# Performance work log

Hardware: AMD Instinct MI355X
Metric: run time of the kernel (lower is better)

## Reference

```python
import jax, jax.numpy as jnp
import numpy as np
from jax import lax

B, N, CIN, MID, OUT, G, H, CHILDS = 16, 1024, 256, 512, 256, 4, 1, 512


def _ln(x, g, b, eps=1e-6):
    m = x.mean(-1, keepdims=True)
    v = ((x - m) ** 2).mean(-1, keepdims=True)
    return (x - m) / jnp.sqrt(v + eps) * g + b


def _gconv(x, W, b):
    # grouped 1x1 conv1d: x [B,Cin,N], W [Cout, Cin//G], b [Cout]
    Bb, Cin, Nn = x.shape
    Cout = W.shape[0]
    xg = x.reshape(Bb, G, Cin // G, Nn)
    Wg = W.reshape(G, Cout // G, Cin // G)
    y = jnp.einsum('bgcn,goc->bgon', xg, Wg).reshape(Bb, Cout, Nn)
    return y + b[None, :, None]


def _forward(x, masks_roi1, masks_roi2, score_mask, gt_feat,
             W_att, b_att, W1, b1, W2, b2, g1, beta1, g2, beta2, Wg, bg):
    dt = x.dtype
    # gt branch
    gts = jax.nn.relu(gt_feat @ Wg + bg)  # [B,N,OUT]

    mr1 = masks_roi1 * score_mask[:, None, :]
    mr2 = masks_roi2 * score_mask[:, None, :]

    # attention logits without materializing the [B,N,N,2C] concat:
    # ft[b,i,j] = cat(x[b,j], x[b,i]);  logits = ft @ W_att + b_att
    Wq, Wk = W_att[:CIN], W_att[CIN:]
    lj = jnp.einsum('bjc,ch->bjh', x, Wq)  # query part (varies over j)
    li = jnp.einsum('bic,ch->bih', x, Wk)  # key part   (varies over i)
    attn = jax.nn.sigmoid(lj[:, None, :, :] + li[:, :, None, :] + b_att)  # [B,N,N,H]

    attn1 = attn * mr1[:, :, :, None]
    attn2 = attn * mr2[:, :, :, None]

    # torch fancy-index assign atten_mask[:,:,idces,:]=1 reduces to: any column
    # index appearing in ANY topk index set gets 1 along dim 2 for all b,i,h.
    k4, k2 = CHILDS // 4, CHILDS // 2
    a1 = jnp.moveaxis(attn1, 2, 3)  # [B,N,H,N] -> topk over last axis (= dim 2)
    a2 = jnp.moveaxis(attn2, 2, 3)
    idx1 = lax.top_k(a1, k4)[1]
    idx1m = lax.top_k(-a1, k4)[1]
    idx2 = lax.top_k(a2, k2)[1]
    idx2m = lax.top_k(-a2, k4)[1]
    all_idx = jnp.concatenate([idx1.ravel(), idx1m.ravel(), idx2.ravel(), idx2m.ravel()])
    col = jnp.zeros((N,), dtype=dt).at[all_idx].set(1.0)

    attn = attn * (mr1 + mr2)[:, :, :, None] * col[None, None, :, None]

    f = (score_mask == 0).astype(dt)  # [B,N]
    f_diag = f[:, :, None] * jnp.eye(N, dtype=dt)  # diag_embed
    atten = (attn + f_diag[:, :, :, None]) / CHILDS
    atten = jnp.transpose(atten, (0, 3, 2, 1))  # [B,H,Nj,Ni]

    x_t = jnp.transpose(x, (0, 2, 1))  # [B,CIN,N]
    o1 = jax.nn.relu(_gconv(x_t, W1, b1))  # [B,MID,N]
    o1m = jnp.matmul(o1.reshape(B, H, MID // H, N), atten).reshape(B, MID, N)
    o1m = _ln(jnp.transpose(o1m, (0, 2, 1)), g1, beta1)  # [B,N,MID]
    o1 = o1 + jnp.transpose(o1m, (0, 2, 1))

    o2 = jax.nn.relu(_gconv(o1, W2, b2))  # [B,OUT,N]
    o2m = jnp.matmul(o2.reshape(B, H, OUT // H, N), atten).reshape(B, OUT, N)
    node_feat = _ln(jnp.transpose(o2m, (0, 2, 1)), g2, beta2)  # [B,N,OUT]
    o2 = o2 + jnp.transpose(node_feat, (0, 2, 1))
    output2 = jnp.transpose(o2, (0, 2, 1))  # [B,N,OUT]
    return output2, gts, node_feat


def setup_inputs() -> dict:
    key = jax.random.key(0)
    ks = jax.random.split(key, 16)
    x = jax.random.normal(ks[0], (B, N, CIN), jnp.float32)
    masks_roi1 = (jax.random.uniform(ks[1], (B, N, N)) < 0.1).astype(jnp.float32)
    masks_roi2 = (jax.random.uniform(ks[2], (B, N, N)) < 0.1).astype(jnp.float32)
    score_mask = (jax.random.uniform(ks[3], (B, N)) < 0.8).astype(jnp.float32)
    gt_feat = jax.random.normal(ks[4], (B, N, CIN), jnp.float32)
    s = 0.05
    W_att = jax.random.normal(ks[5], (2 * CIN, H), jnp.float32) * s
    b_att = jnp.zeros((H,), jnp.float32)
    W1 = jax.random.normal(ks[6], (MID, CIN // G), jnp.float32) * s
    b1 = jax.random.normal(ks[7], (MID,), jnp.float32) * s
    W2 = jax.random.normal(ks[8], (OUT, MID // G), jnp.float32) * s
    b2 = jax.random.normal(ks[9], (OUT,), jnp.float32) * s
    g1 = jax.random.normal(ks[10], (MID,), jnp.float32) * s
    beta1 = jnp.zeros((MID,), jnp.float32)
    g2 = jax.random.normal(ks[11], (OUT,), jnp.float32) * s
    beta2 = jnp.zeros((OUT,), jnp.float32)
    Wg = jax.random.normal(ks[12], (CIN, OUT), jnp.float32) * s
    bg = jax.random.normal(ks[13], (OUT,), jnp.float32) * s
    return {"x": x, "masks_roi1": masks_roi1, "masks_roi2": masks_roi2,
            "score_mask": score_mask, "gt_feat": gt_feat,
            "W_att": W_att, "b_att": b_att, "W1": W1, "b1": b1,
            "W2": W2, "b2": b2, "g1": g1, "beta1": beta1,
            "g2": g2, "beta2": beta2, "Wg": Wg, "bg": bg}


def reference(x, masks_roi1, masks_roi2, score_mask, gt_feat,
              W_att, b_att, W1, b1, W2, b2, g1, beta1, g2, beta2, Wg, bg):
    return _forward(x, masks_roi1, masks_roi2, score_mask, gt_feat,
                    W_att, b_att, W1, b1, W2, b2, g1, beta1, g2, beta2, Wg, bg)
```

## Files before the change

kernel.cpp:

```cpp
#include <hip/hip_runtime.h>
#include <cstddef>
#include <cstdint>

#define B_ 16
#define N_ 1024
#define CIN_ 256
#define MID_ 512
#define OUT_ 256

typedef __attribute__((ext_vector_type(8))) short short8v;
typedef __attribute__((ext_vector_type(4))) float f32x4;
typedef unsigned long long ull;

__device__ __forceinline__ float sigf(float z){ return 1.f/(1.f+expf(-z)); }
__device__ __forceinline__ ushort f2bf(float f){
  uint32_t u=__float_as_uint(f);
  uint32_t r=(u + 0x7fffu + ((u>>16)&1u))>>16;
  return (ushort)r;
}
__device__ __forceinline__ float bf2f(ushort u){ return __uint_as_float(((uint32_t)u)<<16); }

__device__ __forceinline__ void async16(void* lds, const void* g){
  __builtin_amdgcn_global_load_lds(
      (const __attribute__((address_space(1))) uint32_t*)g,
      (__attribute__((address_space(3))) uint32_t*)lds,
      16, 0, 0);
}

__device__ __forceinline__ int colbit(const ull* __restrict__ cm, int j){
  return (int)((cm[((j>>8)<<2) | (j&3)] >> ((j>>2)&63)) & 1ull);
}

__global__ __launch_bounds__(256) void k_pc(const float* __restrict__ x,
    const float* __restrict__ gt, const float* __restrict__ Watt,
    float* __restrict__ lj, float* __restrict__ li,
    ushort* __restrict__ xb, ushort* __restrict__ gtb)
{
  int bid=blockIdx.x, wid=threadIdx.x>>6, lane=threadIdx.x&63;
  if(bid < 4096){
    int row = bid*4 + wid;
    float4 xv = ((const float4*)(x + (size_t)row*CIN_))[lane];
    ((ushort4*)(xb + (size_t)row*CIN_))[lane] =
        make_ushort4(f2bf(xv.x), f2bf(xv.y), f2bf(xv.z), f2bf(xv.w));
    float4 q = ((const float4*)Watt)[lane];
    float4 w = ((const float4*)(Watt + CIN_))[lane];
    float aq = xv.x*q.x+xv.y*q.y+xv.z*q.z+xv.w*q.w;
    float ak = xv.x*w.x+xv.y*w.y+xv.z*w.z+xv.w*w.w;
    #pragma unroll
    for(int off=32; off; off>>=1){ aq += __shfl_xor(aq,off); ak += __shfl_xor(ak,off); }
    if(lane==0){ lj[row]=aq; li[row]=ak; }
  } else {
    int row = (bid-4096)*4 + wid;
    float4 v = ((const float4*)(gt + (size_t)row*CIN_))[lane];
    ((ushort4*)(gtb + (size_t)row*CIN_))[lane] =
        make_ushort4(f2bf(v.x), f2bf(v.y), f2bf(v.z), f2bf(v.w));
  }
}

__global__ __launch_bounds__(256) void k_wcast(const float* __restrict__ W1,
    const float* __restrict__ W2, const float* __restrict__ Wg,
    ushort* __restrict__ W1b, ushort* __restrict__ W2b, ushort* __restrict__ WgTb)
{
  int bid=blockIdx.x, t=threadIdx.x;
  if(bid<128){ int i=bid*256+t; W1b[i]=f2bf(W1[i]); }
  else if(bid<256){ int i=(bid-128)*256+t; W2b[i]=f2bf(W2[i]); }
  else { int idx=(bid-256)*256+t; int o=idx>>8, c=idx&255; WgTb[idx]=f2bf(Wg[(size_t)c*OUT_+o]); }
}

__global__ __launch_bounds__(256) void k_colat(
    const float* __restrict__ m1, const float* __restrict__ m2,
    const float* __restrict__ sc, const float* __restrict__ lj,
    const float* __restrict__ li, const float* __restrict__ batt,
    ushort* __restrict__ Atb, ull* __restrict__ blockmask)
{
  int row = blockIdx.x; int b = row >> 10; int i = row & 1023;
  int t = threadIdx.x, lane = t&63, wid = t>>6;
  size_t base = (size_t)row*N_ + 4*t;
  float4 m1v = *(const float4*)(m1 + base);
  float4 m2v = *(const float4*)(m2 + base);
  float4 scv = *(const float4*)(sc + (b<<10) + 4*t);
  float4 ljv = *(const float4*)(lj + (b<<10) + 4*t);
  float lir = li[row], ba = batt[0];
  float fi = (sc[(b<<10)+i]==0.f)?1.f:0.f;
  float mr1[4] = {m1v.x*scv.x, m1v.y*scv.y, m1v.z*scv.z, m1v.w*scv.w};
  float mr2[4] = {m2v.x*scv.x, m2v.y*scv.y, m2v.z*scv.z, m2v.w*scv.w};
  float ljr[4] = {ljv.x,ljv.y,ljv.z,ljv.w};
  ushort o[4];
  #pragma unroll
  for(int k=0;k<4;++k){
    float v = sigf(ljr[k]+lir+ba);
    float val = v*(mr1[k]+mr2[k]);
    if(4*t+k==i) val += fi;
    o[k] = f2bf(val*(1.f/512.f));
  }
  *(ushort4*)(Atb+base) = make_ushort4(o[0],o[1],o[2],o[3]);
  ull zb1m0=__ballot(mr1[0]==0.f), zb1m1=__ballot(mr1[1]==0.f),
      zb1m2=__ballot(mr1[2]==0.f), zb1m3=__ballot(mr1[3]==0.f);
  ull zb2m0=__ballot(mr2[0]==0.f), zb2m1=__ballot(mr2[1]==0.f),
      zb2m2=__ballot(mr2[2]==0.f), zb2m3=__ballot(mr2[3]==0.f);
  int wz1 = __popcll(zb1m0)+__popcll(zb1m1)+__popcll(zb1m2)+__popcll(zb1m3);
  int wz2 = __popcll(zb2m0)+__popcll(zb2m1)+__popcll(zb2m2)+__popcll(zb2m3);
  __shared__ int wz[8];
  if(lane==0){ wz[wid]=wz1; wz[4+wid]=wz2; }
  __syncthreads();
  int pre1=0, pre2=0, Z1=0, Z2=0;
  #pragma unroll
  for(int w2=0;w2<4;++w2){
    Z1 += wz[w2]; Z2 += wz[4+w2];
    if(w2<wid){ pre1 += wz[w2]; pre2 += wz[4+w2]; }
  }
  ull lt = (1ull<<lane)-1ull;
  int r1 = pre1 + __popcll(zb1m0&lt)+__popcll(zb1m1&lt)+__popcll(zb1m2&lt)+__popcll(zb1m3&lt);
  int r2 = pre2 + __popcll(zb2m0&lt)+__popcll(zb2m1&lt)+__popcll(zb2m2&lt)+__popcll(zb2m3&lt);
  int P1 = 1024-Z1, P2 = 1024-Z2;
  bool rare = (P1>128)||(P2>256)||(Z1<128)||(Z2<128);
  bool q0,q1,q2,q3;
  if(!rare){
    int zb1=r1, zb2=r2;
    q0 = (mr1[0]!=0.f)||(zb1<128)||(mr2[0]!=0.f)||(zb2<128)||(P2+zb2<256);
    zb1 += (int)((zb1m0>>lane)&1ull); zb2 += (int)((zb2m0>>lane)&1ull);
    q1 = (mr1[1]!=0.f)||(zb1<128)||(mr2[1]!=0.f)||(zb2<128)||(P2+zb2<256);
    zb1 += (int)((zb1m1>>lane)&1ull); zb2 += (int)((zb2m1>>lane)&1ull);
    q2 = (mr1[2]!=0.f)||(zb1<128)||(mr2[2]!=0.f)||(zb2<128)||(P2+zb2<256);
    zb1 += (int)((zb1m2>>lane)&1ull); zb2 += (int)((zb2m2>>lane)&1ull);
    q3 = (mr1[3]!=0.f)||(zb1<128)||(mr2[3]!=0.f)||(zb2<128)||(P2+zb2<256);
  } else {
    const float* m1r = m1 + (size_t)row*N_;
    const float* m2r = m2 + (size_t)row*N_;
    const float* scr = sc + (b<<10);
    const float* ljp = lj + (b<<10);
    float a1v[4], a2v[4];
    #pragma unroll
    for(int k=0;k<4;++k){
      float v = sigf(ljp[4*t+k]+lir+ba);
      a1v[k]=mr1[k]*v; a2v[k]=mr2[k]*v;
    }
    int c1[4]={0,0,0,0}, c1m[4]={0,0,0,0}, c2[4]={0,0,0,0}, c2m[4]={0,0,0,0};
    for(int jp=0;jp<N_;++jp){
      float vv = sigf(ljp[jp]+lir+ba);
      float p1 = m1r[jp]*scr[jp]*vv, p2 = m2r[jp]*scr[jp]*vv;
      #pragma unroll
      for(int k=0;k<4;++k){
        bool lo = jp < 4*t+k;
        c1[k] += (p1>a1v[k])||((p1==a1v[k])&&lo);
        c1m[k]+= (p1<a1v[k])||((p1==a1v[k])&&lo);
        c2[k] += (p2>a2v[k])||((p2==a2v[k])&&lo);
        c2m[k]+= (p2<a2v[k])||((p2==a2v[k])&&lo);
      }
    }
    q0 = (c1[0]<128||c1m[0]<128||c2[0]<256||c2m[0]<128);
    q1 = (c1[1]<128||c1m[1]<128||c2[1]<256||c2m[1]<128);
    q2 = (c1[2]<128||c1m[2]<128||c2[2]<256||c2m[2]<128);
    q3 = (c1[3]<128||c1m[3]<128||c2[3]<256||c2m[3]<128);
  }
  ull bq0=__ballot(q0), bq1=__ballot(q1), bq2=__ballot(q2), bq3=__ballot(q3);
  if(lane<4){
    ull v = (lane==0)?bq0 : (lane==1)?bq1 : (lane==2)?bq2 : bq3;
    blockmask[(size_t)(wid*4+lane)*16384 + row] = v;
  }
}

__global__ __launch_bounds__(256) void k_colred(const ull* __restrict__ blockmask,
    ull* __restrict__ colmask64)
{
  int w = blockIdx.x;
  const ull* p = blockmask + (size_t)w*16384;
  ull acc = 0;
  for(int r=threadIdx.x; r<16384; r+=256) acc |= p[r];
  #pragma unroll
  for(int off=32; off; off>>=1) acc |= __shfl_xor(acc, off);
  __shared__ ull sm[4];
  int lane=threadIdx.x&63, wid=threadIdx.x>>6;
  if(lane==0) sm[wid]=acc;
  __syncthreads();
  if(threadIdx.x==0) colmask64[w] = sm[0]|sm[1]|sm[2]|sm[3];
}

template<int BM,int BN,int WR,int WC,int BK>
__global__ __launch_bounds__(256) void mgemm(
    const ushort* __restrict__ A, int lda, long long sAb, long long sAg,
    const ushort* __restrict__ Bp, int ldb, long long sBb, long long sBg,
    float* __restrict__ C, ushort* __restrict__ Cb, int ldc, long long sCb, long long sCg,
    ushort* __restrict__ CbT, long long sTb, long long sTg, int ldt,
    const ull* __restrict__ colmask, int scaleCb,
    const ushort* __restrict__ corrT, long long sQb, int ldq, const float* __restrict__ scp,
    int K, int nG,
    const float* __restrict__ biasM, int biasMG,
    const float* __restrict__ biasN, int relu)
{
  static_assert(WR*WC==4 && BM==WR*64 && BN==WC*64, "tile");
  __shared__ __align__(16) ushort As[BM*BK];
  __shared__ __align__(16) ushort Bs[BN*BK];
  int z=blockIdx.z, b=z/nG, g=z%nG;
  A  += (size_t)b*sAb + (size_t)g*sAg;
  Bp += (size_t)b*sBb + (size_t)g*sBg;
  size_t cOff = (size_t)b*sCb + (size_t)g*sCg;
  size_t tOff = (size_t)b*sTb + (size_t)g*sTg;
  int m0 = blockIdx.y*BM, n0 = blockIdx.x*BN;
  int tid=threadIdx.x, w=tid>>6, lane=tid&63;
  int la=lane&15, hi=lane>>4;
  int wr=w/WC, wc=w%WC;
  f32x4 acc[4][4] = {};
  constexpr int ISS = (BM+BN)*BK/2048;
  for(int k0=0;k0<K;k0+=BK){
    #pragma unroll
    for(int r=0;r<ISS;++r){
      int e = (r*256 + tid)*8;
      if(e < BM*BK){
        int row=e/BK, kk=e%BK;
        async16((char*)As + (size_t)e*2, A + (size_t)(m0+row)*lda + k0+kk);
      } else {
        int e2=e-BM*BK; int row=e2/BK, kk=e2%BK;
        async16((char*)Bs + (size_t)e2*2, Bp + (size_t)(n0+row)*ldb + k0+kk);
      }
    }
    __syncthreads();
    #pragma unroll
    for(int h=0;h<BK/32;++h){
      short8v af[4], bf4[4];
      #pragma unroll
      for(int i2=0;i2<4;++i2) af[i2] = *(const short8v*)&As[(wr*64+i2*16+la)*BK + h*32 + hi*8];
      #pragma unroll
      for(int j2=0;j2<4;++j2) bf4[j2] = *(const short8v*)&Bs[(wc*64+j2*16+la)*BK + h*32 + hi*8];
      #pragma unroll
      for(int i2=0;i2<4;++i2)
        #pragma unroll
        for(int j2=0;j2<4;++j2)
          acc[i2][j2] = __builtin_amdgcn_mfma_f32_16x16x32_bf16(af[i2], bf4[j2], acc[i2][j2], 0,0,0);
    }
    __syncthreads();
  }
  #pragma unroll
  for(int i2=0;i2<4;++i2){
    int row0 = m0 + wr*64 + i2*16 + hi*4;
    #pragma unroll
    for(int j2=0;j2<4;++j2){
      int col = n0 + wc*64 + j2*16 + la;
      float bn = biasN ? biasN[col] : 0.f;
      float cs = (scaleCb && !colbit(colmask, col)) ? 0.f : 1.f;
      #pragma unroll
      for(int r=0;r<4;++r){
        int row = row0 + r;
        float v = acc[i2][j2][r] + bn + (biasM ? biasM[(size_t)g*biasMG + row] : 0.f);
        if(corrT){
          if(scp[(size_t)b*1024 + row]==0.f && !colbit(colmask, row))
            v += (1.f/512.f)*bf2f(corrT[(size_t)b*sQb + (size_t)row*ldq + col]);
        }
        if(relu) v = fmaxf(v, 0.f);
        if(C)   C  [cOff + (size_t)row*ldc + col] = v;
        if(Cb)  Cb [cOff + (size_t)row*ldc + col] = f2bf(v*cs);
        if(CbT) CbT[tOff + (size_t)col*ldt + row] = f2bf(v);
      }
    }
  }
}

__global__ __launch_bounds__(256) void k_ln1(const ushort* __restrict__ o1mTb,
    const ushort* __restrict__ o1bT,
    const float* __restrict__ g1v, const float* __restrict__ be1, ushort* __restrict__ o1pb)
{
  int row=blockIdx.x, t=threadIdx.x;
  ushort2 vv = ((const ushort2*)(o1mTb + (size_t)row*MID_))[t];
  float vx=bf2f(vv.x), vy=bf2f(vv.y);
  float s=vx+vy, s2=vx*vx+vy*vy;
  for(int off=32; off; off>>=1){ s+=__shfl_down(s,off); s2+=__shfl_down(s2,off); }
  __shared__ float sm[8];
  int lane=t&63, wid=t>>6;
  if(lane==0){ sm[wid]=s; sm[4+wid]=s2; }
  __syncthreads();
  s=sm[0]+sm[1]+sm[2]+sm[3]; s2=sm[4]+sm[5]+sm[6]+sm[7];
  float mean=s*(1.f/MID_), var=s2*(1.f/MID_)-mean*mean;
  float rstd=rsqrtf(var+1e-6f);
  int m0=2*t;
  float a0=(vx-mean)*rstd*g1v[m0]+be1[m0];
  float a1=(vy-mean)*rstd*g1v[m0+1]+be1[m0+1];
  ushort2 rr = ((const ushort2*)(o1bT + (size_t)row*MID_))[t];
  ushort2 o; o.x=f2bf(a0+bf2f(rr.x)); o.y=f2bf(a1+bf2f(rr.y));
  ((ushort2*)(o1pb + (size_t)row*MID_))[t] = o;
}

__global__ __launch_bounds__(256) void k_ln2f(const ushort* __restrict__ o2mTb,
    const ushort* __restrict__ o2bT,
    const float* __restrict__ g2v, const float* __restrict__ be2,
    float* __restrict__ node, float* __restrict__ out2)
{
  int row=blockIdx.x, t=threadIdx.x;
  float v = bf2f(o2mTb[(size_t)row*OUT_ + t]);
  float s=v, s2=v*v;
  for(int off=32; off; off>>=1){ s+=__shfl_down(s,off); s2+=__shfl_down(s2,off); }
  __shared__ float sm[8];
  int lane=t&63, wid=t>>6;
  if(lane==0){ sm[wid]=s; sm[4+wid]=s2; }
  __syncthreads();
  s=sm[0]+sm[1]+sm[2]+sm[3]; s2=sm[4]+sm[5]+sm[6]+sm[7];
  float mean=s*(1.f/OUT_); float var=s2*(1.f/OUT_)-mean*mean;
  float rstd=rsqrtf(var+1e-6f);
  float nf=(v-mean)*rstd*g2v[t]+be2[t];
  size_t ro=(size_t)row*OUT_+t;
  node[ro]=nf;
  out2[ro]=nf + bf2f(o2bT[ro]);
}

extern "C" void kernel_launch(void* const* d_in, const int* in_sizes, int n_in,
                              void* d_out, int out_size, void* d_ws, size_t ws_size,
                              hipStream_t stream)
{
  const float* x    = (const float*)d_in[0];
  const float* m1   = (const float*)d_in[1];
  const float* m2   = (const float*)d_in[2];
  const float* sc   = (const float*)d_in[3];
  const float* gt   = (const float*)d_in[4];
  const float* Watt = (const float*)d_in[5];
  const float* batt = (const float*)d_in[6];
  const float* W1   = (const float*)d_in[7];
  const float* b1   = (const float*)d_in[8];
  const float* W2   = (const float*)d_in[9];
  const float* b2   = (const float*)d_in[10];
  const float* g1   = (const float*)d_in[11];
  const float* be1  = (const float*)d_in[12];
  const float* g2   = (const float*)d_in[13];
  const float* be2  = (const float*)d_in[14];
  const float* Wg   = (const float*)d_in[15];
  const float* bg   = (const float*)d_in[16];

  float* out2 = (float*)d_out;
  float* gtso = out2 + (size_t)B_*N_*OUT_;
  float* node = gtso + (size_t)B_*N_*OUT_;

  char* ws = (char*)d_ws;
  float* lj   = (float*)(ws);
  float* li   = (float*)(ws + 65536);
  ushort* W1b = (ushort*)(ws + 131072);
  ushort* W2b = (ushort*)(ws + 196608);
  ushort* WgTb= (ushort*)(ws + 262144);
  ull* colmask= (ull*)(ws + 393216);
  ull* blockmask = (ull*)(ws + 1048576);
  ushort* Atb = (ushort*)(ws + 4194304);
  ushort* xb   = (ushort*)(ws + 37748736);
  ushort* gtb  = (ushort*)(ws + 46137344);
  ushort* o2b  = xb;
  ushort* o2bT = gtb;
  ushort* o1b  = (ushort*)(ws + 54525952);
  ushort* o1pb = o1b;
  ushort* o1bT = (ushort*)(ws + 71303168);
  ushort* o2mTb= (ushort*)(ws + 71303168);
  ushort* o1mTb= (ushort*)(ws + 88080384);

  k_pc    <<<dim3(8192),dim3(256),0,stream>>>(x, gt, Watt, lj, li, xb, gtb);
  k_wcast <<<dim3(512),dim3(256),0,stream>>>(W1, W2, Wg, W1b, W2b, WgTb);
  k_colat <<<dim3(B_*N_),dim3(256),0,stream>>>(m1,m2,sc,lj,li,batt,Atb,blockmask);
  k_colred<<<dim3(16),dim3(256),0,stream>>>(blockmask, colmask);

  mgemm<128,128,2,2,64><<<dim3(2,128,1),256,0,stream>>>(
      gtb, CIN_, 0,0,
      WgTb, CIN_, 0,0,
      gtso, (ushort*)0, OUT_, 0,0,
      (ushort*)0, 0,0,0,
      (ull*)0, 0, (ushort*)0, 0,0, (float*)0,
      CIN_, 1, nullptr,0, bg, 1);

  mgemm<128,128,2,2,64><<<dim3(8,1,B_*4),256,0,stream>>>(
      W1b, 64, 0, (long long)128*64,
      xb, CIN_, (long long)N_*CIN_, 64,
      (float*)0, o1b, N_, (long long)MID_*N_, (long long)128*N_,
      o1bT, (long long)N_*MID_, 128, MID_,
      colmask, 1, (ushort*)0, 0,0, (float*)0,
      64, 4, b1, 128, nullptr, 1);

  mgemm<128,128,2,2,64><<<dim3(4,8,B_),256,0,stream>>>(
      Atb, N_, (long long)N_*N_, 0,
      o1b, N_, (long long)MID_*N_, 0,
      (float*)0, o1mTb, MID_, (long long)N_*MID_, 0,
      (ushort*)0, 0,0,0,
      colmask, 0, o1bT, (long long)N_*MID_, MID_, sc,
      N_, 1, nullptr,0, nullptr, 0);

  k_ln1<<<dim3(B_*N_),256,0,stream>>>(o1mTb, o1bT, g1, be1, o1pb);

  mgemm<64,256,1,4,64><<<dim3(4,1,B_*4),256,0,stream>>>(
      W2b, 128, 0, (long long)64*128,
      o1pb, MID_, (long long)N_*MID_, 128,
      (float*)0, o2b, N_, (long long)OUT_*N_, (long long)64*N_,
      o2bT, (long long)N_*OUT_, 64, OUT_,
      colmask, 1, (ushort*)0, 0,0, (float*)0,
      128, 4, b2, 64, nullptr, 1);

  mgemm<128,128,2,2,64><<<dim3(2,8,B_),256,0,stream>>>(
      Atb, N_, (long long)N_*N_, 0,
      o2b, N_, (long long)OUT_*N_, 0,
      (float*)0, o2mTb, OUT_, (long long)N_*OUT_, 0,
      (ushort*)0, 0,0,0,
      colmask, 0, o2bT, (long long)N_*OUT_, OUT_, sc,
      N_, 1, nullptr,0, nullptr, 0);

  k_ln2f<<<dim3(B_*N_),256,0,stream>>>(o2mTb, o2bT, g2, be2, node, out2);
}
```

Before: 425.5 us.

## Stage transposed GEMM stores through LDS and precompute column/row correction factors

The transposed bf16 output of the two grouped-conv GEMMs is now staged in shared memory and written out as coalesced 16-byte rows, replacing strided 2-byte scatter stores. A small kernel precomputes per-column scale and per-row correction factors so the GEMM epilogue skips bitmask decoding and the conditional corrT reads. The sigmoid also uses hardware exp2/rcp intrinsics. This adds a launch and an extra sync, and uses more LDS in the transposing variants.

```diff
diff --git a/kernel.cpp b/kernel.cpp
--- a/kernel.cpp
+++ b/kernel.cpp
@@ -12,7 +12,10 @@
 typedef __attribute__((ext_vector_type(4))) float f32x4;
 typedef unsigned long long ull;
 
-__device__ __forceinline__ float sigf(float z){ return 1.f/(1.f+expf(-z)); }
+__device__ __forceinline__ float sigf(float z){
+  float e = __builtin_amdgcn_exp2f(-z*1.44269504f);
+  return __builtin_amdgcn_rcpf(1.f+e);
+}
 __device__ __forceinline__ ushort f2bf(float f){
   uint32_t u=__float_as_uint(f);
   uint32_t r=(u + 0x7fffu + ((u>>16)&1u))>>16;
@@ -176,21 +179,36 @@
   if(threadIdx.x==0) colmask64[w] = sm[0]|sm[1]|sm[2]|sm[3];
 }
 
-template<int BM,int BN,int WR,int WC,int BK>
+__global__ __launch_bounds__(256) void k_fcorr(const ull* __restrict__ colmask,
+    const float* __restrict__ sc, float* __restrict__ fcorr, float* __restrict__ colscale)
+{
+  int i = blockIdx.x*256 + threadIdx.x;
+  int j = i & 1023;
+  int cb = colbit(colmask, j);
+  fcorr[i] = (sc[i]==0.f && !cb) ? (1.f/512.f) : 0.f;
+  if(i < 1024) colscale[i] = cb ? 1.f : 0.f;
+}
+
+template<int BM,int BN,int WR,int WC,int BK,int TRT>
 __global__ __launch_bounds__(256) void mgemm(
     const ushort* __restrict__ A, int lda, long long sAb, long long sAg,
     const ushort* __restrict__ Bp, int ldb, long long sBb, long long sBg,
     float* __restrict__ C, ushort* __restrict__ Cb, int ldc, long long sCb, long long sCg,
-    ushort* __restrict__ CbT, long long sTb, long long sTg, int ldt,
-    const ull* __restrict__ colmask, int scaleCb,
-    const ushort* __restrict__ corrT, long long sQb, int ldq, const float* __restrict__ scp,
+    ushort* __restrict__ CbT, long long sTb, long long sTg, int ldtg,
+    const float* __restrict__ colscale,
+    const float* __restrict__ fcorr,
+    const ushort* __restrict__ corrT, long long sQb, int ldq,
     int K, int nG,
     const float* __restrict__ biasM, int biasMG,
     const float* __restrict__ biasN, int relu)
 {
   static_assert(WR*WC==4 && BM==WR*64 && BN==WC*64, "tile");
-  __shared__ __align__(16) ushort As[BM*BK];
-  __shared__ __align__(16) ushort Bs[BN*BK];
+  constexpr int STG = (BM+BN)*BK;
+  constexpr int LDT = BM + 8;
+  constexpr int SH  = (TRT && (BN*LDT) > STG) ? (BN*LDT) : STG;
+  __shared__ __align__(16) ushort Sh[SH];
+  ushort* As = Sh;
+  ushort* Bs = Sh + BM*BK;
   int z=blockIdx.z, b=z/nG, g=z%nG;
   A  += (size_t)b*sAb + (size_t)g*sAg;
   Bp += (size_t)b*sBb + (size_t)g*sBg;
@@ -230,27 +248,50 @@
     }
     __syncthreads();
   }
+  int colL[4]; float bnv[4], csv[4];
+  #pragma unroll
+  for(int j2=0;j2<4;++j2){
+    colL[j2] = wc*64 + j2*16 + la;
+    int col = n0 + colL[j2];
+    bnv[j2] = biasN ? biasN[col] : 0.f;
+    csv[j2] = colscale ? colscale[col] : 1.f;
+  }
   #pragma unroll
   for(int i2=0;i2<4;++i2){
-    int row0 = m0 + wr*64 + i2*16 + hi*4;
+    int rowB = wr*64 + i2*16 + hi*4;
+    float bmv[4], fcv[4];
+    #pragma unroll
+    for(int r=0;r<4;++r){
+      int row = m0 + rowB + r;
+      bmv[r] = biasM ? biasM[(size_t)g*biasMG + row] : 0.f;
+      fcv[r] = fcorr ? fcorr[(size_t)b*1024 + row] : 0.f;
+    }
     #pragma unroll
     for(int j2=0;j2<4;++j2){
-      int col = n0 + wc*64 + j2*16 + la;
-      float bn = biasN ? biasN[col] : 0.f;
-      float cs = (scaleCb && !colbit(colmask, col)) ? 0.f : 1.f;
+      int col = n0 + colL[j2];
+      ushort pk[4];
       #pragma unroll
       for(int r=0;r<4;++r){
-        int row = row0 + r;
-        float v = acc[i2][j2][r] + bn + (biasM ? biasM[(size_t)g*biasMG + row] : 0.f);
-        if(corrT){
-          if(scp[(size_t)b*1024 + row]==0.f && !colbit(colmask, row))
-            v += (1.f/512.f)*bf2f(corrT[(size_t)b*sQb + (size_t)row*ldq + col]);
-        }
-        if(relu) v = fmaxf(v, 0.f);
-        if(C)   C  [cOff + (size_t)row*ldc + col] = v;
-        if(Cb)  Cb [cOff + (size_t)row*ldc + col] = f2bf(v*cs);
-        if(CbT) CbT[tOff + (size_t)col*ldt + row] = f2bf(v);
+        int row = m0 + rowB + r;
+        float v = acc[i2][j2][r] + bnv[j2] + bmv[r];
+        if(corrT && fcv[r]!=0.f)
+          v += fcv[r]*bf2f(corrT[(size_t)b*sQb + (size_t)row*ldq + col]);
+        if(relu) v = fmaxf(v,0.f);
+        if(C)  C [cOff + (size_t)row*ldc + col] = v;
+        if(Cb) Cb[cOff + (size_t)row*ldc + col] = f2bf(v*csv[j2]);
+        if(TRT) pk[r] = f2bf(v);
       }
+      if(TRT) *(ushort4*)&Sh[(size_t)colL[j2]*LDT + rowB] = make_ushort4(pk[0],pk[1],pk[2],pk[3]);
+    }
+  }
+  if(TRT){
+    __syncthreads();
+    #pragma unroll
+    for(int u=0;u<BM*BN/2048;++u){
+      int idx = u*256 + tid;
+      int col = idx/(BM/8), r8 = idx%(BM/8);
+      short8v vv = *(const short8v*)&Sh[(size_t)col*LDT + r8*8];
+      *(short8v*)(CbT + tOff + (size_t)(n0+col)*ldtg + m0 + r8*8) = vv;
     }
   }
 }
@@ -328,14 +369,16 @@
   float* node = gtso + (size_t)B_*N_*OUT_;
 
   char* ws = (char*)d_ws;
-  float* lj   = (float*)(ws);
-  float* li   = (float*)(ws + 65536);
-  ushort* W1b = (ushort*)(ws + 131072);
-  ushort* W2b = (ushort*)(ws + 196608);
-  ushort* WgTb= (ushort*)(ws + 262144);
-  ull* colmask= (ull*)(ws + 393216);
+  float* lj    = (float*)(ws);
+  float* li    = (float*)(ws + 65536);
+  ushort* W1b  = (ushort*)(ws + 131072);
+  ushort* W2b  = (ushort*)(ws + 196608);
+  ushort* WgTb = (ushort*)(ws + 262144);
+  ull* colmask = (ull*)(ws + 393216);
+  float* colscale = (float*)(ws + 397312);
+  float* fcorr = (float*)(ws + 401408);
   ull* blockmask = (ull*)(ws + 1048576);
-  ushort* Atb = (ushort*)(ws + 4194304);
+  ushort* Atb  = (ushort*)(ws + 4194304);
   ushort* xb   = (ushort*)(ws + 37748736);
   ushort* gtb  = (ushort*)(ws + 46137344);
   ushort* o2b  = xb;
@@ -350,47 +393,48 @@
   k_wcast <<<dim3(512),dim3(256),0,stream>>>(W1, W2, Wg, W1b, W2b, WgTb);
   k_colat <<<dim3(B_*N_),dim3(256),0,stream>>>(m1,m2,sc,lj,li,batt,Atb,blockmask);
   k_colred<<<dim3(16),dim3(256),0,stream>>>(blockmask, colmask);
-
-  mgemm<128,128,2,2,64><<<dim3(2,128,1),256,0,stream>>>(
+  k_fcorr <<<dim3(64),dim3(256),0,stream>>>(colmask, sc, fcorr, colscale);
+
+  mgemm<128,128,2,2,64,0><<<dim3(2,128,1),256,0,stream>>>(
       gtb, CIN_, 0,0,
       WgTb, CIN_, 0,0,
       gtso, (ushort*)0, OUT_, 0,0,
       (ushort*)0, 0,0,0,
-      (ull*)0, 0, (ushort*)0, 0,0, (float*)0,
+      nullptr, nullptr, (ushort*)0, 0,0,
       CIN_, 1, nullptr,0, bg, 1);
 
-  mgemm<128,128,2,2,64><<<dim3(8,1,B_*4),256,0,stream>>>(
+  mgemm<128,128,2,2,64,1><<<dim3(8,1,B_*4),256,0,stream>>>(
       W1b, 64, 0, (long long)128*64,
       xb, CIN_, (long long)N_*CIN_, 64,
       (float*)0, o1b, N_, (long long)MID_*N_, (long long)128*N_,
       o1bT, (long long)N_*MID_, 128, MID_,
-      colmask, 1, (ushort*)0, 0,0, (float*)0,
+      colscale, nullptr, (ushort*)0, 0,0,
       64, 4, b1, 128, nullptr, 1);
 
-  mgemm<128,128,2,2,64><<<dim3(4,8,B_),256,0,stream>>>(
+  mgemm<128,128,2,2,64,0><<<dim3(4,8,B_),256,0,stream>>>(
       Atb, N_, (long long)N_*N_, 0,
       o1b, N_, (long long)MID_*N_, 0,
       (float*)0, o1mTb, MID_, (long long)N_*MID_, 0,
       (ushort*)0, 0,0,0,
-      colmask, 0, o1bT, (long long)N_*MID_, MID_, sc,
+      nullptr, fcorr, o1bT, (long long)N_*MID_, MID_,
       N_, 1, nullptr,0, nullptr, 0);
 
   k_ln1<<<dim3(B_*N_),256,0,stream>>>(o1mTb, o1bT, g1, be1, o1pb);
 
-  mgemm<64,256,1,4,64><<<dim3(4,1,B_*4),256,0,stream>>>(
+  mgemm<64,256,1,4,64,1><<<dim3(4,1,B_*4),256,0,stream>>>(
       W2b, 128, 0, (long long)64*128,
       o1pb, MID_, (long long)N_*MID_, 128,
       (float*)0, o2b, N_, (long long)OUT_*N_, (long long)64*N_,
       o2bT, (long long)N_*OUT_, 64, OUT_,
-      colmask, 1, (ushort*)0, 0,0, (float*)0,
+      colscale, nullptr, (ushort*)0, 0,0,
       128, 4, b2, 64, nullptr, 1);
 
-  mgemm<128,128,2,2,64><<<dim3(2,8,B_),256,0,stream>>>(
+  mgemm<128,128,2,2,64,0><<<dim3(2,8,B_),256,0,stream>>>(
       Atb, N_, (long long)N_*N_, 0,
       o2b, N_, (long long)OUT_*N_, 0,
       (float*)0, o2mTb, OUT_, (long long)N_*OUT_, 0,
       (ushort*)0, 0,0,0,
-      colmask, 0, o2bT, (long long)N_*OUT_, OUT_, sc,
+      nullptr, fcorr, o2bT, (long long)N_*OUT_, OUT_,
       N_, 1, nullptr,0, nullptr, 0);
 
   k_ln2f<<<dim3(B_*N_),256,0,stream>>>(o2mTb, o2bT, g2, be2, node, out2);
```

Measured after the change: 381.2 us. -10.4%, faster.
